# Kernel optimization log

Hardware: AMD Instinct MI355X
Metric: run time of the kernel (lower is better)

The kernel has to match this reference:

```python
import jax, jax.numpy as jnp
import numpy as np

B, T, C, H, W = 16, 8, 16, 64, 64
HID = 32          # round(sqrt(num_audio_input_ch * num_latent_ch)) = sqrt(16*64)
LAT = 64          # num_latent_ch
K = 3             # kernel_size


def conv(x, w, b):
    # x: [B,Cin,H,W], w: [Cout,Cin,K,K] (OIHW), SAME padding == padding (1,1) for 3x3
    y = jax.lax.conv_general_dilated(x, w, (1, 1), 'SAME',
                                     dimension_numbers=('NCHW', 'OIHW', 'NCHW'))
    return y + b[None, :, None, None]


def lstm_scan(x_seq, w, b, hid):
    # x_seq: [T,B,Cin,H,W] -> hidden sequence [T,B,hid,H,W]
    Bn, Hh, Ww = x_seq.shape[1], x_seq.shape[3], x_seq.shape[4]
    h0 = jnp.zeros((Bn, hid, Hh, Ww), x_seq.dtype)

    def step(carry, x_t):
        h, c = carry
        z = conv(jnp.concatenate([x_t, h], axis=1), w, b)     # [B,4*hid,H,W]
        i, f, o, g = jnp.split(z, 4, axis=1)                   # gate order i,f,o,g
        c2 = jax.nn.sigmoid(f) * c + jax.nn.sigmoid(i) * jnp.tanh(g)
        h2 = jax.nn.sigmoid(o) * jnp.tanh(c2)
        return (h2, c2), h2

    _, hs = jax.lax.scan(step, (h0, h0), x_seq)
    return hs


def bidir_layer(x_seq, wf, bf, wb, bb, hid):
    hf = lstm_scan(x_seq, wf, bf, hid)
    hb = jnp.flip(lstm_scan(jnp.flip(x_seq, 0), wb, bb, hid), 0)
    return jnp.concatenate([hf, hb], axis=2)                   # [T,B,2*hid,H,W]


def setup_inputs() -> dict:
    key = jax.random.key(0)
    ks = jax.random.split(key, 16)
    s = 0.05
    pe_dim = C * H * W
    inp = {
        'x_audio': jax.random.normal(ks[0], (B, T, C, H, W), jnp.float32),
        'midi_notes': jax.random.uniform(ks[1], (B, T, 2), jnp.float32, 0.0, 127.0),
        # note encoder: Linear(2,4) -> ReLU -> Linear(4, C*H*W) -> Tanh
        'enc_w1': jax.random.normal(ks[2], (2, 4), jnp.float32) * s,
        'enc_b1': jnp.zeros((4,), jnp.float32),
        'enc_w2': jax.random.normal(ks[3], (4, pe_dim), jnp.float32) * s,
        'enc_b2': jnp.zeros((pe_dim,), jnp.float32),
        # layer 0 (input C=16), fwd + bwd cells
        'w0f': jax.random.normal(ks[4], (4 * HID, C + HID, K, K), jnp.float32) * s,
        'b0f': jnp.zeros((4 * HID,), jnp.float32),
        'w0b': jax.random.normal(ks[5], (4 * HID, C + HID, K, K), jnp.float32) * s,
        'b0b': jnp.zeros((4 * HID,), jnp.float32),
        # layer 1 (input 2*HID=64)
        'w1f': jax.random.normal(ks[6], (4 * HID, 2 * HID + HID, K, K), jnp.float32) * s,
        'b1f': jnp.zeros((4 * HID,), jnp.float32),
        'w1b': jax.random.normal(ks[7], (4 * HID, 2 * HID + HID, K, K), jnp.float32) * s,
        'b1b': jnp.zeros((4 * HID,), jnp.float32),
        # final conv: 2*HID -> LAT
        'fc_w': jax.random.normal(ks[8], (LAT, 2 * HID, K, K), jnp.float32) * s,
        'fc_b': jnp.zeros((LAT,), jnp.float32),
    }
    return inp


def reference(x_audio, midi_notes, enc_w1, enc_b1, enc_w2, enc_b2,
              w0f, b0f, w0b, b0b, w1f, b1f, w1b, b1b, fc_w, fc_b):
    # positional encoding from MIDI notes, vectorized over all timesteps
    notes = -0.5 + midi_notes / 64.0                              # [B,T,2]
    pe = jnp.tanh(jax.nn.relu(notes @ enc_w1 + enc_b1) @ enc_w2 + enc_b2)  # [B,T,C*H*W]
    x = x_audio + pe.reshape(x_audio.shape)
    xs = jnp.transpose(x, (1, 0, 2, 3, 4))                        # [T,B,C,H,W]
    h = bidir_layer(xs, w0f, b0f, w0b, b0b, HID)                  # [T,B,64,H,W]
    h = bidir_layer(h, w1f, b1f, w1b, b1b, HID)                   # [T,B,64,H,W]
    return conv(h[-1], fc_w, fc_b)                                # [B,LAT,H,W]
```

## Files before the change

kernel.cpp:

```cpp
#include <hip/hip_runtime.h>

typedef _Float16 f16;
typedef _Float16 f16x8 __attribute__((ext_vector_type(8)));
typedef float f32x16 __attribute__((ext_vector_type(16)));

namespace {

constexpr int B_ = 16, T_ = 8, HW = 4096;

__device__ __forceinline__ float sigm(float x)  { return 1.f / (1.f + __expf(-x)); }
__device__ __forceinline__ float ftanh(float x) { return 1.f - 2.f / (1.f + __expf(2.f * x)); }

__device__ __forceinline__ f32x16 zero16() {
  f32x16 v;
#pragma unroll
  for (int i = 0; i < 16; ++i) v[i] = 0.f;
  return v;
}

__device__ __forceinline__ f16x8 zero8h() {
  f16x8 v;
#pragma unroll
  for (int i = 0; i < 8; ++i) v[i] = (f16)0.f;
  return v;
}

struct WSet { const float* src; f16* dst; int KC, NCO, CIN; };

__global__ void warr_kernel(WSet s0, WSet s1, WSet s2, WSet s3, WSet s4) {
  WSet s = s0;
  switch (blockIdx.y) { case 1: s = s1; break; case 2: s = s2; break;
                        case 3: s = s3; break; case 4: s = s4; break; default: break; }
  int n = 9 * s.KC * s.NCO * 16;
  int i = blockIdx.x * 256 + threadIdx.x;
  if (i >= n) return;
  int kk = i & 15;
  int t = i >> 4;
  int co = t % s.NCO;
  int dkc = t / s.NCO;
  int kc = dkc % s.KC, dydx = dkc / s.KC;
  int ci = kc * 16 + kk;
  float v = (ci < s.CIN) ? s.src[(co * s.CIN + ci) * 9 + dydx] : 0.f;
  s.dst[i] = (f16)v;
}

__global__ void pe_kernel(const float* __restrict__ xa, const float* __restrict__ midi,
                          const float* __restrict__ w1, const float* __restrict__ b1,
                          const float* __restrict__ w2, const float* __restrict__ b2,
                          f16* __restrict__ xs) {
  int gid = blockIdx.x * 256 + threadIdx.x;
  int half = gid & 1;
  int gpx = gid >> 1;
  int bt = gpx >> 12, gp = gpx & 4095;
  float n0 = -0.5f + midi[bt * 2 + 0] * (1.f / 64.f);
  float n1 = -0.5f + midi[bt * 2 + 1] * (1.f / 64.f);
  float hk[4];
#pragma unroll
  for (int k = 0; k < 4; ++k)
    hk[k] = fmaxf(fmaf(n0, w1[k], fmaf(n1, w1[4 + k], b1[k])), 0.f);
  f16x8 ov;
#pragma unroll
  for (int j = 0; j < 8; ++j) {
    int c = half * 8 + j;
    long p = (long)c * HW + gp;
    float z = b2[p];
#pragma unroll
    for (int k = 0; k < 4; ++k) z = fmaf(hk[k], w2[(long)k * 65536 + p], z);
    ov[j] = (f16)(xa[(long)bt * 65536 + p] + ftanh(z));
  }
  *reinterpret_cast<f16x8*>(xs + (long)gpx * 16 + half * 8) = ov;
}

struct ConvDir {
  const f16* x;  long xbs;
  const f16* h;  long hbs;
  const f16* w;
  const float* bias;
  const float* cin;
  float* cout;
  f16* hout; long hobs;
};

template<int CIN1, int CIN2, int CINPAD, int KCF, int KC, int CH, int HST, int HOST,
         bool GATES, int NCO, int MG, int MFRAG>
__global__ __launch_bounds__(512, 4)
void conv_mfma(ConvDir p0, ConvDir p1)
{
  constexpr int NG = 8 / MG;
  constexpr int NCH = KC / CH;
  constexpr int NPH = 9 * NCH;
  constexpr int ACT_BYTES = 180 * CINPAD * 2;
  constexpr int ZB_BYTES  = GATES ? 128 * 128 * 2 : 0;
  constexpr int SMEM = ACT_BYTES > ZB_BYTES ? ACT_BYTES : ZB_BYTES;
  __shared__ __align__(16) char smem[SMEM];
  f16* act = (f16*)smem;
  f16* zls = (f16*)smem;

  const ConvDir P = blockIdx.y ? p1 : p0;
  const int b = blockIdx.z;
  const int tileY = blockIdx.x >> 2, tileX = blockIdx.x & 3;
  const int gy0 = tileY * 8, gx0 = tileX * 16;
  const int tid = threadIdx.x;

  const int lane = tid & 63, wv = tid >> 6;
  const int mg = wv % MG, ng = wv / MG;
  const int rl = lane & 31;
  const int khalf = (lane >> 5) * 8;
  const int laneA = ((rl >> 4) * 18 + (rl & 15)) * CINPAD + khalf;
  const int laneB = rl * 16 + khalf;
  const f16* __restrict__ wng = P.w + laneB + (long)ng * 32 * 16;
  const f16* __restrict__ arow = act + laneA;

  constexpr int UPX = CIN1 / 8, UPH = CIN2 / 8, UPP = UPX + UPH;
  constexpr int NU  = 180 * UPP;
  constexpr int PER = (NU + 511) / 512;
  const bool have_h = (P.h != nullptr);
  f16x8 sreg[PER];
#pragma unroll
  for (int p = 0; p < PER; ++p) {
    sreg[p] = zero8h();
    int i = tid + p * 512;
    if (i < NU) {
      int px = i / UPP, u = i - px * UPP;
      int py = px / 18, pxx = px - py * 18;
      int gy = gy0 + py - 1, gx = gx0 + pxx - 1;
      if ((unsigned)gy < 64u && (unsigned)gx < 64u && (u < UPX || have_h)) {
        long gp = (long)gy * 64 + gx;
        const f16* src = (u < UPX) ? (P.x + b * P.xbs + gp * CIN1 + u * 8)
                                   : (P.h + b * P.hbs + gp * HST + (u - UPX) * 8);
        sreg[p] = *reinterpret_cast<const f16x8*>(src);
      }
    }
  }

  f16x8 bfr[2][CH];
  f16x8 afr[2][MFRAG][CH];

  auto LBF = [&](int ph) {
    const int slot = ph & 1;
    const int dydx = ph / NCH, kc0 = (ph % NCH) * CH;
#pragma unroll
    for (int c = 0; c < CH; ++c)
      bfr[slot][c] = *reinterpret_cast<const f16x8*>(
          wng + (long)(dydx * KCF + kc0 + c) * NCO * 16);
  };
  auto LAF = [&](int ph) {
    const int slot = ph & 1;
    const int dydx = ph / NCH, kc0 = (ph % NCH) * CH;
    const int dy = dydx / 3, dx = dydx % 3;
#pragma unroll
    for (int m = 0; m < MFRAG; ++m)
#pragma unroll
      for (int c = 0; c < CH; ++c)
        afr[slot][m][c] = *reinterpret_cast<const f16x8*>(
            arow + dx * CINPAD + (((mg * MFRAG + m) * 2 + dy) * 18) * CINPAD
            + (kc0 + c) * 16);
  };

  LBF(0);
  if (NPH > 1) LBF(1);

#pragma unroll
  for (int p = 0; p < PER; ++p) {
    int i = tid + p * 512;
    if (i < NU) {
      int px = i / UPP, u = i - px * UPP;
      *reinterpret_cast<f16x8*>(act + px * CINPAD + u * 8) = sreg[p];
    }
  }
  __syncthreads();

  f32x16 acc[MFRAG];
#pragma unroll
  for (int m = 0; m < MFRAG; ++m) acc[m] = zero16();

  LAF(0);
#pragma unroll
  for (int ph = 0; ph < NPH; ++ph) {
    const int slot = ph & 1;
    if (ph + 1 < NPH) LAF(ph + 1);
#pragma unroll
    for (int c = 0; c < CH; ++c)
#pragma unroll
      for (int m = 0; m < MFRAG; ++m)
        acc[m] = __builtin_amdgcn_mfma_f32_32x32x16_f16(afr[slot][m][c], bfr[slot][c], acc[m], 0, 0, 0);
    if (ph + 2 < NPH) LBF(ph + 2);
  }

  __syncthreads();

  if constexpr (GATES) {
    const int col = ng * 32 + rl;
    const float bs = P.bias[col];
#pragma unroll
    for (int m = 0; m < MFRAG; ++m) {
#pragma unroll
      for (int r = 0; r < 16; ++r) {
        int row = (r & 3) + 8 * (r >> 2) + 4 * (lane >> 5);
        int px = (mg * MFRAG + m) * 32 + row;
        zls[px * 128 + col] = (f16)(acc[m][r] + bs);
      }
    }
    __syncthreads();
#pragma unroll
    for (int i = 0; i < 8; ++i) {
      int idx = tid + i * 512;
      int hid = idx & 31, px = idx >> 5;
      float zi = (float)zls[px * 128 + hid];
      float zf = (float)zls[px * 128 + 32 + hid];
      float zo = (float)zls[px * 128 + 64 + hid];
      float zg = (float)zls[px * 128 + 96 + hid];
      int py = px >> 4, pxx = px & 15;
      long gp = (long)(gy0 + py) * 64 + (gx0 + pxx);
      long cidx = ((long)b * HW + gp) * 32 + hid;
      float cp = P.cin ? P.cin[cidx] : 0.f;
      float c2 = sigm(zf) * cp + sigm(zi) * ftanh(zg);
      P.cout[cidx] = c2;
      P.hout[b * P.hobs + gp * HOST + hid] = (f16)(sigm(zo) * ftanh(c2));
    }
  } else {
    const int co = ng * 32 + rl;
    const float bs = P.bias[co];
#pragma unroll
    for (int m = 0; m < MFRAG; ++m) {
#pragma unroll
      for (int r = 0; r < 16; ++r) {
        int row = (r & 3) + 8 * (r >> 2) + 4 * (lane >> 5);
        int pxt = (mg * MFRAG + m) * 32 + row;
        int py = pxt >> 4, pxx = pxt & 15;
        long gp = (long)(gy0 + py) * 64 + (gx0 + pxx);
        P.cout[((long)b * NCO + co) * HW + gp] = acc[m][r] + bs;
      }
    }
  }
}

}

extern "C" void kernel_launch(void* const* d_in, const int* in_sizes, int n_in,
                              void* d_out, int out_size, void* d_ws, size_t ws_size,
                              hipStream_t stream) {
  const float* x_audio = (const float*)d_in[0];
  const float* midi    = (const float*)d_in[1];
  const float* enc_w1  = (const float*)d_in[2];
  const float* enc_b1  = (const float*)d_in[3];
  const float* enc_w2  = (const float*)d_in[4];
  const float* enc_b2  = (const float*)d_in[5];
  const float* w0f = (const float*)d_in[6];
  const float* b0f = (const float*)d_in[7];
  const float* w0b = (const float*)d_in[8];
  const float* b0b = (const float*)d_in[9];
  const float* w1f = (const float*)d_in[10];
  const float* b1f = (const float*)d_in[11];
  const float* w1b = (const float*)d_in[12];
  const float* b1b = (const float*)d_in[13];
  const float* fcw = (const float*)d_in[14];
  const float* fcb = (const float*)d_in[15];

  char* ws = (char*)d_ws;
  size_t off = 0;
  auto alloc = [&](size_t bytes) { char* p = ws + off; off += (bytes + 255) & ~(size_t)255; return p; };

  f16* xs    = (f16*)alloc((size_t)B_ * T_ * HW * 16 * 2);
  f16* seq0  = (f16*)alloc((size_t)T_ * B_ * HW * 64 * 2);
  float* c0f = (float*)alloc((size_t)B_ * HW * 32 * 4);
  float* c0b = (float*)alloc((size_t)B_ * HW * 32 * 4);
  float* c1f = (float*)alloc((size_t)B_ * HW * 32 * 4);
  float* c1bw= (float*)alloc((size_t)B_ * HW * 32 * 4);
  f16* h1p0  = (f16*)alloc((size_t)B_ * HW * 32 * 2);
  f16* h1p1  = (f16*)alloc((size_t)B_ * HW * 32 * 2);
  f16* h1bw  = (f16*)alloc((size_t)B_ * HW * 32 * 2);
  f16* wt0f  = (f16*)alloc((size_t)9 * 3 * 128 * 16 * 2);
  f16* wt0b  = (f16*)alloc((size_t)9 * 3 * 128 * 16 * 2);
  f16* wt1f  = (f16*)alloc((size_t)9 * 6 * 128 * 16 * 2);
  f16* wt1b  = (f16*)alloc((size_t)9 * 6 * 128 * 16 * 2);
  f16* wtfc  = (f16*)alloc((size_t)9 * 4 * 64 * 16 * 2);

  {
    WSet s0{w0f, wt0f, 3, 128, 48}, s1{w0b, wt0b, 3, 128, 48};
    WSet s2{w1f, wt1f, 6, 128, 96}, s3{w1b, wt1b, 6, 128, 96};
    WSet s4{fcw, wtfc, 4, 64, 64};
    warr_kernel<<<dim3(432, 5), 256, 0, stream>>>(s0, s1, s2, s3, s4);
  }

  pe_kernel<<<(B_ * T_ * HW * 2) / 256, 256, 0, stream>>>(
      x_audio, midi, enc_w1, enc_b1, enc_w2, enc_b2, xs);

  const long XSB  = (long)T_ * HW * 16;
  const long SLAB = (long)B_ * HW * 64;
  const long SB   = (long)HW * 64;
  const long HB   = (long)HW * 32;

  {
    ConvDir f{xs, XSB, nullptr, SB, wt0f, b0f, nullptr, c0f, seq0, SB};
    ConvDir r{xs + (long)7 * HW * 16, XSB, nullptr, SB, wt0b, b0b, nullptr, c0b,
              seq0 + (long)7 * SLAB + 32, SB};
    conv_mfma<16, 32, 56, 3, 1, 1, 64, 64, true, 128, 2, 2>
        <<<dim3(32, 2, 16), 512, 0, stream>>>(f, r);
  }
  for (int s = 1; s < 8; ++s) {
    int tf = s, tb = 7 - s;
    ConvDir f{xs + (long)tf * HW * 16, XSB,
              seq0 + (long)(tf - 1) * SLAB, SB,
              wt0f, b0f, c0f, c0f,
              seq0 + (long)tf * SLAB, SB};
    ConvDir r{xs + (long)tb * HW * 16, XSB,
              seq0 + (long)(tb + 1) * SLAB + 32, SB,
              wt0b, b0b, c0b, c0b,
              seq0 + (long)tb * SLAB + 32, SB};
    conv_mfma<16, 32, 56, 3, 3, 3, 64, 64, true, 128, 2, 2>
        <<<dim3(32, 2, 16), 512, 0, stream>>>(f, r);
  }

  {
    ConvDir f{seq0, SB, nullptr, HB, wt1f, b1f, nullptr, c1f, h1p0, HB};
    ConvDir r{seq0 + 7 * SLAB, SB, nullptr, HB, wt1b, b1b, nullptr, c1bw, h1bw, HB};
    conv_mfma<64, 32, 104, 6, 4, 2, 32, 32, true, 128, 2, 2>
        <<<dim3(32, 2, 16), 512, 0, stream>>>(f, r);
  }
  for (int s = 1; s < 8; ++s) {
    f16* hprev = (s & 1) ? h1p0 : h1p1;
    f16* hcur  = (s & 1) ? h1p1 : h1p0;
    ConvDir f{seq0 + (long)s * SLAB, SB, hprev, HB, wt1f, b1f, c1f, c1f, hcur, HB};
    conv_mfma<64, 32, 104, 6, 6, 3, 32, 32, true, 128, 2, 2>
        <<<dim3(32, 1, 16), 512, 0, stream>>>(f, f);
  }

  {
    ConvDir f{h1p1, HB, h1bw, HB, wtfc, fcb, nullptr, (float*)d_out, nullptr, 0};
    conv_mfma<32, 32, 72, 4, 4, 2, 32, 32, false, 64, 4, 1>
        <<<dim3(32, 1, 16), 512, 0, stream>>>(f, f);
  }
}
```

Baseline: 499.4 us.

## Store LSTM cell state in fp16, remap MFMA tiling, vectorize gate epilogue

Cell state buffers change from fp32 to fp16, which halves their read and write traffic. Writes of the cell state on the final timestep, and for the unused backward layer-1 cell, are skipped. The MFMA wave tiling changes from splitting over M fragments to splitting over N fragments (MG=4, NF per wave), so each A fragment is reused across output columns. The gate epilogue is vectorized to 8 hidden channels per thread. Keeping the cell state in fp16 across timesteps adds accumulated rounding error.

```diff
diff --git a/kernel.cpp b/kernel.cpp
--- a/kernel.cpp
+++ b/kernel.cpp
@@ -76,19 +76,20 @@
   const f16* h;  long hbs;
   const f16* w;
   const float* bias;
-  const float* cin;
-  float* cout;
+  const f16* cin;
+  f16* cout;
+  float* fout;
   f16* hout; long hobs;
 };
 
-template<int CIN1, int CIN2, int CINPAD, int KCF, int KC, int CH, int HST, int HOST,
-         bool GATES, int NCO, int MG, int MFRAG>
+template<int CIN1, int CIN2, int CINPAD, int KCF, int KC, int HST, int HOST,
+         bool GATES, int NCO, int MG>
 __global__ __launch_bounds__(512, 4)
 void conv_mfma(ConvDir p0, ConvDir p1)
 {
   constexpr int NG = 8 / MG;
-  constexpr int NCH = KC / CH;
-  constexpr int NPH = 9 * NCH;
+  constexpr int NF = NCO / (NG * 32);
+  constexpr int NPH = 9 * KC;
   constexpr int ACT_BYTES = 180 * CINPAD * 2;
   constexpr int ZB_BYTES  = GATES ? 128 * 128 * 2 : 0;
   constexpr int SMEM = ACT_BYTES > ZB_BYTES ? ACT_BYTES : ZB_BYTES;
@@ -108,7 +109,7 @@
   const int khalf = (lane >> 5) * 8;
   const int laneA = ((rl >> 4) * 18 + (rl & 15)) * CINPAD + khalf;
   const int laneB = rl * 16 + khalf;
-  const f16* __restrict__ wng = P.w + laneB + (long)ng * 32 * 16;
+  const f16* __restrict__ wng = P.w + laneB + (long)ng * NF * 32 * 16;
   const f16* __restrict__ arow = act + laneA;
 
   constexpr int UPX = CIN1 / 8, UPH = CIN2 / 8, UPP = UPX + UPH;
@@ -133,28 +134,23 @@
     }
   }
 
-  f16x8 bfr[2][CH];
-  f16x8 afr[2][MFRAG][CH];
+  f16x8 bfr[2][NF];
+  f16x8 afr[2];
 
   auto LBF = [&](int ph) {
     const int slot = ph & 1;
-    const int dydx = ph / NCH, kc0 = (ph % NCH) * CH;
-#pragma unroll
-    for (int c = 0; c < CH; ++c)
-      bfr[slot][c] = *reinterpret_cast<const f16x8*>(
-          wng + (long)(dydx * KCF + kc0 + c) * NCO * 16);
+    const int dydx = ph / KC, kc = ph % KC;
+#pragma unroll
+    for (int nf = 0; nf < NF; ++nf)
+      bfr[slot][nf] = *reinterpret_cast<const f16x8*>(
+          wng + ((long)(dydx * KCF + kc) * NCO + nf * 32) * 16);
   };
   auto LAF = [&](int ph) {
     const int slot = ph & 1;
-    const int dydx = ph / NCH, kc0 = (ph % NCH) * CH;
+    const int dydx = ph / KC, kc = ph % KC;
     const int dy = dydx / 3, dx = dydx % 3;
-#pragma unroll
-    for (int m = 0; m < MFRAG; ++m)
-#pragma unroll
-      for (int c = 0; c < CH; ++c)
-        afr[slot][m][c] = *reinterpret_cast<const f16x8*>(
-            arow + dx * CINPAD + (((mg * MFRAG + m) * 2 + dy) * 18) * CINPAD
-            + (kc0 + c) * 16);
+    afr[slot] = *reinterpret_cast<const f16x8*>(
+        arow + dx * CINPAD + ((mg * 2 + dy) * 18) * CINPAD + kc * 16);
   };
 
   LBF(0);
@@ -170,9 +166,9 @@
   }
   __syncthreads();
 
-  f32x16 acc[MFRAG];
-#pragma unroll
-  for (int m = 0; m < MFRAG; ++m) acc[m] = zero16();
+  f32x16 acc[NF];
+#pragma unroll
+  for (int nf = 0; nf < NF; ++nf) acc[nf] = zero16();
 
   LAF(0);
 #pragma unroll
@@ -180,56 +176,57 @@
     const int slot = ph & 1;
     if (ph + 1 < NPH) LAF(ph + 1);
 #pragma unroll
-    for (int c = 0; c < CH; ++c)
-#pragma unroll
-      for (int m = 0; m < MFRAG; ++m)
-        acc[m] = __builtin_amdgcn_mfma_f32_32x32x16_f16(afr[slot][m][c], bfr[slot][c], acc[m], 0, 0, 0);
+    for (int nf = 0; nf < NF; ++nf)
+      acc[nf] = __builtin_amdgcn_mfma_f32_32x32x16_f16(afr[slot], bfr[slot][nf], acc[nf], 0, 0, 0);
     if (ph + 2 < NPH) LBF(ph + 2);
   }
 
   __syncthreads();
 
   if constexpr (GATES) {
-    const int col = ng * 32 + rl;
-    const float bs = P.bias[col];
-#pragma unroll
-    for (int m = 0; m < MFRAG; ++m) {
+#pragma unroll
+    for (int nf = 0; nf < NF; ++nf) {
+      const int col = (ng * NF + nf) * 32 + rl;
+      const float bs = P.bias[col];
 #pragma unroll
       for (int r = 0; r < 16; ++r) {
         int row = (r & 3) + 8 * (r >> 2) + 4 * (lane >> 5);
-        int px = (mg * MFRAG + m) * 32 + row;
-        zls[px * 128 + col] = (f16)(acc[m][r] + bs);
+        zls[(mg * 32 + row) * 128 + col] = (f16)(acc[nf][r] + bs);
       }
     }
     __syncthreads();
-#pragma unroll
-    for (int i = 0; i < 8; ++i) {
-      int idx = tid + i * 512;
-      int hid = idx & 31, px = idx >> 5;
-      float zi = (float)zls[px * 128 + hid];
-      float zf = (float)zls[px * 128 + 32 + hid];
-      float zo = (float)zls[px * 128 + 64 + hid];
-      float zg = (float)zls[px * 128 + 96 + hid];
-      int py = px >> 4, pxx = px & 15;
-      long gp = (long)(gy0 + py) * 64 + (gx0 + pxx);
-      long cidx = ((long)b * HW + gp) * 32 + hid;
-      float cp = P.cin ? P.cin[cidx] : 0.f;
-      float c2 = sigm(zf) * cp + sigm(zi) * ftanh(zg);
-      P.cout[cidx] = c2;
-      P.hout[b * P.hobs + gp * HOST + hid] = (f16)(sigm(zo) * ftanh(c2));
-    }
+    const int q = tid & 3, px = tid >> 2;
+    const int py = px >> 4, pxx = px & 15;
+    const long gp = (long)(gy0 + py) * 64 + (gx0 + pxx);
+    const f16* zb = zls + px * 128 + q * 8;
+    f16x8 zi8 = *reinterpret_cast<const f16x8*>(zb);
+    f16x8 zf8 = *reinterpret_cast<const f16x8*>(zb + 32);
+    f16x8 zo8 = *reinterpret_cast<const f16x8*>(zb + 64);
+    f16x8 zg8 = *reinterpret_cast<const f16x8*>(zb + 96);
+    const long cbase = ((long)b * HW + gp) * 32 + q * 8;
+    f16x8 c8 = P.cin ? *reinterpret_cast<const f16x8*>(P.cin + cbase) : zero8h();
+    f16x8 c2v, h2v;
+#pragma unroll
+    for (int j = 0; j < 8; ++j) {
+      float c2 = sigm((float)zf8[j]) * (float)c8[j]
+               + sigm((float)zi8[j]) * ftanh((float)zg8[j]);
+      c2v[j] = (f16)c2;
+      h2v[j] = (f16)(sigm((float)zo8[j]) * ftanh(c2));
+    }
+    if (P.cout) *reinterpret_cast<f16x8*>(P.cout + cbase) = c2v;
+    *reinterpret_cast<f16x8*>(P.hout + b * P.hobs + gp * HOST + q * 8) = h2v;
   } else {
-    const int co = ng * 32 + rl;
-    const float bs = P.bias[co];
-#pragma unroll
-    for (int m = 0; m < MFRAG; ++m) {
+#pragma unroll
+    for (int nf = 0; nf < NF; ++nf) {
+      const int co = (ng * NF + nf) * 32 + rl;
+      const float bs = P.bias[co];
 #pragma unroll
       for (int r = 0; r < 16; ++r) {
         int row = (r & 3) + 8 * (r >> 2) + 4 * (lane >> 5);
-        int pxt = (mg * MFRAG + m) * 32 + row;
+        int pxt = mg * 32 + row;
         int py = pxt >> 4, pxx = pxt & 15;
         long gp = (long)(gy0 + py) * 64 + (gx0 + pxx);
-        P.cout[((long)b * NCO + co) * HW + gp] = acc[m][r] + bs;
+        P.fout[((long)b * NCO + co) * HW + gp] = acc[nf][r] + bs;
       }
     }
   }
@@ -263,10 +260,9 @@
 
   f16* xs    = (f16*)alloc((size_t)B_ * T_ * HW * 16 * 2);
   f16* seq0  = (f16*)alloc((size_t)T_ * B_ * HW * 64 * 2);
-  float* c0f = (float*)alloc((size_t)B_ * HW * 32 * 4);
-  float* c0b = (float*)alloc((size_t)B_ * HW * 32 * 4);
-  float* c1f = (float*)alloc((size_t)B_ * HW * 32 * 4);
-  float* c1bw= (float*)alloc((size_t)B_ * HW * 32 * 4);
+  f16* c0f   = (f16*)alloc((size_t)B_ * HW * 32 * 2);
+  f16* c0b   = (f16*)alloc((size_t)B_ * HW * 32 * 2);
+  f16* c1f   = (f16*)alloc((size_t)B_ * HW * 32 * 2);
   f16* h1p0  = (f16*)alloc((size_t)B_ * HW * 32 * 2);
   f16* h1p1  = (f16*)alloc((size_t)B_ * HW * 32 * 2);
   f16* h1bw  = (f16*)alloc((size_t)B_ * HW * 32 * 2);
@@ -292,43 +288,44 @@
   const long HB   = (long)HW * 32;
 
   {
-    ConvDir f{xs, XSB, nullptr, SB, wt0f, b0f, nullptr, c0f, seq0, SB};
+    ConvDir f{xs, XSB, nullptr, SB, wt0f, b0f, nullptr, c0f, nullptr, seq0, SB};
     ConvDir r{xs + (long)7 * HW * 16, XSB, nullptr, SB, wt0b, b0b, nullptr, c0b,
-              seq0 + (long)7 * SLAB + 32, SB};
-    conv_mfma<16, 32, 56, 3, 1, 1, 64, 64, true, 128, 2, 2>
+              nullptr, seq0 + (long)7 * SLAB + 32, SB};
+    conv_mfma<16, 32, 56, 3, 1, 64, 64, true, 128, 4>
         <<<dim3(32, 2, 16), 512, 0, stream>>>(f, r);
   }
   for (int s = 1; s < 8; ++s) {
     int tf = s, tb = 7 - s;
     ConvDir f{xs + (long)tf * HW * 16, XSB,
               seq0 + (long)(tf - 1) * SLAB, SB,
-              wt0f, b0f, c0f, c0f,
+              wt0f, b0f, c0f, (s == 7) ? nullptr : c0f, nullptr,
               seq0 + (long)tf * SLAB, SB};
     ConvDir r{xs + (long)tb * HW * 16, XSB,
               seq0 + (long)(tb + 1) * SLAB + 32, SB,
-              wt0b, b0b, c0b, c0b,
+              wt0b, b0b, c0b, (s == 7) ? nullptr : c0b, nullptr,
               seq0 + (long)tb * SLAB + 32, SB};
-    conv_mfma<16, 32, 56, 3, 3, 3, 64, 64, true, 128, 2, 2>
+    conv_mfma<16, 32, 56, 3, 3, 64, 64, true, 128, 4>
         <<<dim3(32, 2, 16), 512, 0, stream>>>(f, r);
   }
 
   {
-    ConvDir f{seq0, SB, nullptr, HB, wt1f, b1f, nullptr, c1f, h1p0, HB};
-    ConvDir r{seq0 + 7 * SLAB, SB, nullptr, HB, wt1b, b1b, nullptr, c1bw, h1bw, HB};
-    conv_mfma<64, 32, 104, 6, 4, 2, 32, 32, true, 128, 2, 2>
+    ConvDir f{seq0, SB, nullptr, HB, wt1f, b1f, nullptr, c1f, nullptr, h1p0, HB};
+    ConvDir r{seq0 + 7 * SLAB, SB, nullptr, HB, wt1b, b1b, nullptr, nullptr, nullptr, h1bw, HB};
+    conv_mfma<64, 32, 104, 6, 4, 32, 32, true, 128, 4>
         <<<dim3(32, 2, 16), 512, 0, stream>>>(f, r);
   }
   for (int s = 1; s < 8; ++s) {
     f16* hprev = (s & 1) ? h1p0 : h1p1;
     f16* hcur  = (s & 1) ? h1p1 : h1p0;
-    ConvDir f{seq0 + (long)s * SLAB, SB, hprev, HB, wt1f, b1f, c1f, c1f, hcur, HB};
-    conv_mfma<64, 32, 104, 6, 6, 3, 32, 32, true, 128, 2, 2>
+    ConvDir f{seq0 + (long)s * SLAB, SB, hprev, HB, wt1f, b1f,
+              c1f, (s == 7) ? nullptr : c1f, nullptr, hcur, HB};
+    conv_mfma<64, 32, 104, 6, 6, 32, 32, true, 128, 4>
         <<<dim3(32, 1, 16), 512, 0, stream>>>(f, f);
   }
 
   {
-    ConvDir f{h1p1, HB, h1bw, HB, wtfc, fcb, nullptr, (float*)d_out, nullptr, 0};
-    conv_mfma<32, 32, 72, 4, 4, 2, 32, 32, false, 64, 4, 1>
+    ConvDir f{h1p1, HB, h1bw, HB, wtfc, fcb, nullptr, nullptr, (float*)d_out, nullptr, 0};
+    conv_mfma<32, 32, 72, 4, 4, 32, 32, false, 64, 4>
         <<<dim3(32, 1, 16), 512, 0, stream>>>(f, f);
   }
 }
```

New measurement: 490.6 us. No clear change (-1.8%).
